# Performance work log

Hardware: AMD Instinct MI355X
Metric: run time of the kernel (lower is better)

Reference implementation:

```python
import jax, jax.numpy as jnp
import numpy as np

N_NODES = 50000
N_EDGES = 1600000
D_FEAT = 512
FILTERS = 256
NUM_CLASSES = 16


def setup_inputs() -> dict:
    key = jax.random.key(0)
    k = jax.random.split(key, 6)
    x = jax.random.normal(k[0], (N_NODES, D_FEAT), dtype=jnp.float32)
    W1 = jax.random.normal(k[1], (D_FEAT, FILTERS), dtype=jnp.float32) * (1.0 / np.sqrt(D_FEAT))
    W2 = jax.random.normal(k[2], (FILTERS, NUM_CLASSES), dtype=jnp.float32) * (1.0 / np.sqrt(FILTERS))
    edge_weight = jax.random.uniform(k[3], (N_EDGES,), dtype=jnp.float32)
    edge_src = jax.random.randint(k[4], (N_EDGES,), 0, N_NODES, dtype=jnp.int32)
    edge_dst = jax.random.randint(k[5], (N_EDGES,), 0, N_NODES, dtype=jnp.int32)
    return {"x": x, "W1": W1, "W2": W2, "edge_weight": edge_weight,
            "edge_src": edge_src, "edge_dst": edge_dst}


def _propagate(h, edge_src, edge_dst, edge_weight):
    # sparse A @ h: out[dst] += w * h[src]
    msgs = edge_weight[:, None] * h[edge_src]          # [E, F]
    return jax.ops.segment_sum(msgs, edge_dst, num_segments=N_NODES)


def reference(x, W1, W2, edge_weight, edge_src, edge_dst):
    # Dropout layers are identity at inference (training=False).
    # Layer 1: relu(A @ (X @ W1))
    h = jax.nn.relu(_propagate(x @ W1, edge_src, edge_dst, edge_weight))
    # Layer 2: softmax(A @ (H @ W2))
    logits = _propagate(h @ W2, edge_src, edge_dst, edge_weight)
    return jax.nn.softmax(logits, axis=-1)
```

## Files before the change

kernel.cpp:

```cpp
#include <hip/hip_runtime.h>

#define N_NODES 50000
#define N_EDGES 1600000
#define D_FEAT 512
#define FILTERS 256
#define NUM_CLASSES 16
#define NXCD 8

typedef __bf16 bf16x8 __attribute__((ext_vector_type(8)));
typedef float f32x4 __attribute__((ext_vector_type(4)));
typedef _Float16 half4 __attribute__((ext_vector_type(4)));
typedef _Float16 f16x8 __attribute__((ext_vector_type(8)));

#define GLOAD_LDS16(g, l)                                                  \
  __builtin_amdgcn_global_load_lds(                                        \
      (const __attribute__((address_space(1))) unsigned int*)(g),          \
      (__attribute__((address_space(3))) unsigned int*)(l), 16, 0, 0)

__global__ __launch_bounds__(256) void hist8_kernel(
    const int* __restrict__ edst, int* __restrict__ deg8) {
  const int e = blockIdx.x * 256 + threadIdx.x;
  if (e >= N_EDGES) return;
  const int x = blockIdx.x & (NXCD - 1);
  atomicAdd(&deg8[x * N_NODES + edst[e]], 1);
}

#define SCAN_NB 196
__global__ __launch_bounds__(256) void scan_blocks_kernel(
    const int* __restrict__ deg8, int* __restrict__ row_ptr,
    int* __restrict__ bsum, const float* __restrict__ W1,
    __bf16* __restrict__ Wth, __bf16* __restrict__ Wtl) {
  const int gtid = blockIdx.x * 256 + threadIdx.x;
  for (int i = gtid; i < D_FEAT * FILTERS; i += SCAN_NB * 256) {
    const float v = W1[i];
    const int k = i >> 8;
    const int n = i & 255;
    const __bf16 h = (__bf16)v;
    Wth[n * D_FEAT + k] = h;
    Wtl[n * D_FEAT + k] = (__bf16)(v - (float)h);
  }

  __shared__ int s[256];
  const int i = gtid;
  int v = 0;
  if (i < N_NODES) {
#pragma unroll
    for (int x = 0; x < NXCD; ++x) v += deg8[x * N_NODES + i];
  }
  s[threadIdx.x] = v;
  __syncthreads();
  for (int off = 1; off < 256; off <<= 1) {
    const int t = (threadIdx.x >= off) ? s[threadIdx.x - off] : 0;
    __syncthreads();
    s[threadIdx.x] += t;
    __syncthreads();
  }
  if (i < N_NODES) row_ptr[i] = s[threadIdx.x] - v;
  if (threadIdx.x == 255) bsum[blockIdx.x] = s[255];
}

__global__ __launch_bounds__(256) void scan_add_cursor8_kernel(
    int* __restrict__ row_ptr, const int* __restrict__ bsum,
    const int* __restrict__ deg8, int* __restrict__ cursor8) {
  __shared__ int wsum[4];
  const int lane = threadIdx.x & 63;
  const int wave = threadIdx.x >> 6;
  int v = (threadIdx.x < blockIdx.x) ? bsum[threadIdx.x] : 0;
#pragma unroll
  for (int off = 32; off >= 1; off >>= 1) v += __shfl_xor(v, off, 64);
  if (lane == 0) wsum[wave] = v;
  __syncthreads();
  const int boff = wsum[0] + wsum[1] + wsum[2] + wsum[3];

  const int i = blockIdx.x * 256 + threadIdx.x;
  if (i < N_NODES) {
    int run = row_ptr[i] + boff;
    row_ptr[i] = run;
#pragma unroll
    for (int x = 0; x < NXCD; ++x) {
      cursor8[x * N_NODES + i] = run;
      run += deg8[x * N_NODES + i];
    }
  }
  if (i == 0) row_ptr[N_NODES] = N_EDGES;
}

__global__ __launch_bounds__(256) void fill8_kernel(
    const int* __restrict__ esrc, const int* __restrict__ edst,
    const float* __restrict__ ew, int* __restrict__ cursor8,
    uint2* __restrict__ meta8) {
  const int e = blockIdx.x * 256 + threadIdx.x;
  if (e >= N_EDGES) return;
  const int x = blockIdx.x & (NXCD - 1);
  const int d = edst[e];
  const int pos = atomicAdd(&cursor8[x * N_NODES + d], 1);
  meta8[pos] = make_uint2((unsigned)esrc[e] | ((unsigned)(d & 15) << 16),
                          __float_as_uint(ew[e]));
}

__global__ __launch_bounds__(256) void gemm1_mfma_kernel(
    const float* __restrict__ A, const __bf16* __restrict__ Bh,
    const __bf16* __restrict__ Bl, _Float16* __restrict__ C) {
  const int K = D_FEAT;
  __shared__ __bf16 sAh[128 * 32];
  __shared__ __bf16 sAl[128 * 32];
  __shared__ __bf16 sBh[128 * 32];
  __shared__ __bf16 sBl[128 * 32];

  const int tid = threadIdx.x;
  const int wave = tid >> 6;
  const int lane = tid & 63;
  const int wm = (wave >> 1) * 64;
  const int wn = (wave & 1) * 64;
  const int m0 = blockIdx.x * 128;
  const int n0 = blockIdx.y * 128;

  const int arow = tid >> 1;
  const int aks = (tid & 1) * 16;
  int am = m0 + arow;
  if (am >= N_NODES) am = N_NODES - 1;
  const float* aptr = A + (size_t)am * K + aks;

  const int lr = lane >> 2;
  const int lc = (lane & 3) * 8;
  const int fm = lane & 15;
  const int fq = lane >> 4;

  f32x4 acc[4][4] = {};

  for (int k0 = 0; k0 < K; k0 += 32) {
    const float4* ap = (const float4*)(aptr + k0);
    const float4 a0 = ap[0], a1 = ap[1], a2 = ap[2], a3 = ap[3];

    __syncthreads();

#pragma unroll
    for (int i = 0; i < 2; ++i) {
      const int row = wave * 32 + i * 16;
      GLOAD_LDS16(Bh + (size_t)(n0 + row + lr) * K + k0 + lc, sBh + row * 32);
      GLOAD_LDS16(Bl + (size_t)(n0 + row + lr) * K + k0 + lc, sBl + row * 32);
    }

    float va[16] = {a0.x, a0.y, a0.z, a0.w, a1.x, a1.y, a1.z, a1.w,
                    a2.x, a2.y, a2.z, a2.w, a3.x, a3.y, a3.z, a3.w};
    __bf16 hh[16], ll[16];
#pragma unroll
    for (int i = 0; i < 16; ++i) {
      const __bf16 h = (__bf16)va[i];
      hh[i] = h;
      ll[i] = (__bf16)(va[i] - (float)h);
    }
    *(bf16x8*)(sAh + arow * 32 + aks) = *(bf16x8*)&hh[0];
    *(bf16x8*)(sAh + arow * 32 + aks + 8) = *(bf16x8*)&hh[8];
    *(bf16x8*)(sAl + arow * 32 + aks) = *(bf16x8*)&ll[0];
    *(bf16x8*)(sAl + arow * 32 + aks + 8) = *(bf16x8*)&ll[8];

    __syncthreads();

    bf16x8 fah[4], fal[4], fbh[4], fbl[4];
#pragma unroll
    for (int t = 0; t < 4; ++t) {
      const int moff = (wm + t * 16 + fm) * 32 + fq * 8;
      fah[t] = *(const bf16x8*)(sAh + moff);
      fal[t] = *(const bf16x8*)(sAl + moff);
      const int noff = (wn + t * 16 + fm) * 32 + fq * 8;
      fbh[t] = *(const bf16x8*)(sBh + noff);
      fbl[t] = *(const bf16x8*)(sBl + noff);
    }
#pragma unroll
    for (int i = 0; i < 4; ++i)
#pragma unroll
      for (int j = 0; j < 4; ++j)
        acc[i][j] = __builtin_amdgcn_mfma_f32_16x16x32_bf16(fah[i], fbh[j],
                                                            acc[i][j], 0, 0, 0);
#pragma unroll
    for (int i = 0; i < 4; ++i)
#pragma unroll
      for (int j = 0; j < 4; ++j)
        acc[i][j] = __builtin_amdgcn_mfma_f32_16x16x32_bf16(fah[i], fbl[j],
                                                            acc[i][j], 0, 0, 0);
#pragma unroll
    for (int i = 0; i < 4; ++i)
#pragma unroll
      for (int j = 0; j < 4; ++j)
        acc[i][j] = __builtin_amdgcn_mfma_f32_16x16x32_bf16(fal[i], fbh[j],
                                                            acc[i][j], 0, 0, 0);
  }

#pragma unroll
  for (int ti = 0; ti < 4; ++ti) {
#pragma unroll
    for (int r = 0; r < 4; ++r) {
      const int m = m0 + wm + ti * 16 + fq * 4 + r;
      if (m < N_NODES) {
#pragma unroll
        for (int tj = 0; tj < 4; ++tj) {
          const int n = n0 + wn + tj * 16 + fm;
          C[(size_t)m * FILTERS + n] = (_Float16)acc[ti][tj][r];
        }
      }
    }
  }
}

__global__ __launch_bounds__(256) void gather1_gemm2_kernel(
    const _Float16* __restrict__ xw1, const int* __restrict__ row_ptr,
    const uint2* __restrict__ meta8, const float* __restrict__ W2,
    _Float16* __restrict__ h2) {
  __shared__ float red[4][16][17];
  const int wave = threadIdx.x >> 6;
  const int lane = threadIdx.x & 63;
  const int node = blockIdx.x * 4 + wave;
  const int beg = row_ptr[node];
  const int end = row_ptr[node + 1];

  float acc[4] = {};
  const half4* __restrict__ xw1v = (const half4*)xw1;

  for (int c0 = beg; c0 < end; c0 += 64) {
    const int cnt = min(64, end - c0);
    const uint2 mv = meta8[c0 + ((lane < cnt) ? lane : 0)];

    for (int j = 0; j < cnt; j += 8) {
      int srcs[8];
      float ws[8];
#pragma unroll
      for (int u = 0; u < 8; ++u) {
        const int live = (j + u < cnt);
        const int l = live ? (j + u) : 0;
        srcs[u] = __builtin_amdgcn_readlane((int)mv.x, l) & 0xFFFF;
        const int wb = __builtin_amdgcn_readlane((int)mv.y, l);
        ws[u] = live ? __int_as_float(wb) : 0.f;
      }
      half4 v[8];
#pragma unroll
      for (int u = 0; u < 8; ++u)
        v[u] = xw1v[(unsigned)srcs[u] * 64u + (unsigned)lane];
#pragma unroll
      for (int u = 0; u < 8; ++u)
#pragma unroll
        for (int i = 0; i < 4; ++i)
          acc[i] = fmaf(ws[u], (float)v[u][i], acc[i]);
    }
  }

  float r[4];
#pragma unroll
  for (int i = 0; i < 4; ++i) r[i] = fmaxf(acc[i], 0.f);

  float p[16] = {};
#pragma unroll
  for (int j = 0; j < 4; ++j) {
    const float4* wr = (const float4*)(W2 + (size_t)(lane * 4 + j) * NUM_CLASSES);
#pragma unroll
    for (int c4 = 0; c4 < 4; ++c4) {
      const float4 wv = wr[c4];
      p[c4 * 4 + 0] = fmaf(r[j], wv.x, p[c4 * 4 + 0]);
      p[c4 * 4 + 1] = fmaf(r[j], wv.y, p[c4 * 4 + 1]);
      p[c4 * 4 + 2] = fmaf(r[j], wv.z, p[c4 * 4 + 2]);
      p[c4 * 4 + 3] = fmaf(r[j], wv.w, p[c4 * 4 + 3]);
    }
  }

#pragma unroll
  for (int off = 32; off >= 16; off >>= 1)
#pragma unroll
    for (int i = 0; i < 16; ++i) p[i] += __shfl_xor(p[i], off, 64);

  if (lane < 16) {
#pragma unroll
    for (int i = 0; i < 16; ++i) red[wave][lane][i] = p[i];
  }
  if (lane < 16) {
    float sum = 0.f;
#pragma unroll
    for (int i = 0; i < 16; ++i) sum += red[wave][i][lane];
    h2[(size_t)node * NUM_CLASSES + lane] = (_Float16)sum;
  }
}

__global__ __launch_bounds__(256) void gather2_mfma_kernel(
    const _Float16* __restrict__ h2, const int* __restrict__ row_ptr,
    const uint2* __restrict__ meta8, float* __restrict__ out) {
  __shared__ _Float16 lds[4][16][72];
  const int wave = threadIdx.x >> 6;
  const int lane = threadIdx.x & 63;
  const int tile = blockIdx.x * 4 + wave;
  if (tile >= N_NODES / 16) return;
  const int t0 = tile * 16;
  const int beg = row_ptr[t0];
  const int end = row_ptr[t0 + 16];

  const int cls = lane & 15;
  const int kq = lane >> 4;
  const int erow = lane >> 1;
  const int part = lane & 1;

  f32x4 acc = {0.f, 0.f, 0.f, 0.f};
  _Float16* myl = &lds[wave][0][0];

  if (beg < end) {
    const int last = end - 1;
    int e = beg + lane;
    uint2 m = meta8[(e <= last) ? e : last];
    float wv = (e <= last) ? __uint_as_float(m.y) : 0.f;

    for (int c0 = beg; c0 < end; c0 += 64) {
      uint2 mn = m;
      float wn = 0.f;
      const int c1 = c0 + 64;
      if (c1 < end) {
        const int en = c1 + lane;
        mn = meta8[(en <= last) ? en : last];
        wn = (en <= last) ? __uint_as_float(mn.y) : 0.f;
      }

      const int se0 = __shfl((int)m.x, erow, 64) & 0xFFFF;
      const int se1 = __shfl((int)m.x, 32 + erow, 64) & 0xFFFF;
      const f16x8 r0 =
          *(const f16x8*)(h2 + (size_t)se0 * NUM_CLASSES + part * 8);
      const f16x8 r1 =
          *(const f16x8*)(h2 + (size_t)se1 * NUM_CLASSES + part * 8);

      f16x8 a0, a1;
#pragma unroll
      for (int j = 0; j < 8; ++j) {
        const int ei = kq * 8 + j;
        const int p0 = __shfl((int)m.x, ei, 64);
        const float w0 = __shfl(wv, ei, 64);
        a0[j] = (((p0 >> 16) & 15) == cls) ? (_Float16)w0 : (_Float16)0.f;
        const int p1 = __shfl((int)m.x, 32 + ei, 64);
        const float w1 = __shfl(wv, 32 + ei, 64);
        a1[j] = (((p1 >> 16) & 15) == cls) ? (_Float16)w1 : (_Float16)0.f;
      }

#pragma unroll
      for (int j = 0; j < 8; ++j) myl[(part * 8 + j) * 72 + erow] = r0[j];
#pragma unroll
      for (int j = 0; j < 8; ++j) myl[(part * 8 + j) * 72 + 32 + erow] = r1[j];

      const f16x8 b0 = *(const f16x8*)(myl + cls * 72 + kq * 8);
      const f16x8 b1 = *(const f16x8*)(myl + cls * 72 + 32 + kq * 8);

      acc = __builtin_amdgcn_mfma_f32_16x16x32_f16(a0, b0, acc, 0, 0, 0);
      acc = __builtin_amdgcn_mfma_f32_16x16x32_f16(a1, b1, acc, 0, 0, 0);

      m = mn;
      wv = wn;
    }
  }

#pragma unroll
  for (int r = 0; r < 4; ++r) {
    const float a = acc[r];
    float mx = a;
#pragma unroll
    for (int off = 8; off >= 1; off >>= 1)
      mx = fmaxf(mx, __shfl_xor(mx, off, 16));
    const float ex = __expf(a - mx);
    float sm = ex;
#pragma unroll
    for (int off = 8; off >= 1; off >>= 1) sm += __shfl_xor(sm, off, 16);
    out[(size_t)(t0 + kq * 4 + r) * NUM_CLASSES + cls] = ex / sm;
  }
}

extern "C" void kernel_launch(void* const* d_in, const int* in_sizes, int n_in,
                              void* d_out, int out_size, void* d_ws,
                              size_t ws_size, hipStream_t stream) {
  const float* x = (const float*)d_in[0];
  const float* W1 = (const float*)d_in[1];
  const float* W2 = (const float*)d_in[2];
  const float* ew = (const float*)d_in[3];
  const int* esrc = (const int*)d_in[4];
  const int* edst = (const int*)d_in[5];
  float* out = (float*)d_out;

  _Float16* xw1 = (_Float16*)d_ws;
  _Float16* h2 = xw1 + (size_t)N_NODES * FILTERS;
  int* row_ptr = (int*)(h2 + (size_t)N_NODES * NUM_CLASSES);
  int* deg8 = row_ptr + (N_NODES + 1);
  int* cursor8 = deg8 + NXCD * N_NODES;
  uint2* meta8 = (uint2*)(((uintptr_t)(cursor8 + NXCD * N_NODES) + 15) &
                          ~(uintptr_t)15);
  __bf16* w1th = (__bf16*)(meta8 + N_EDGES);
  __bf16* w1tl = w1th + D_FEAT * FILTERS;
  int* bsum = (int*)(w1tl + D_FEAT * FILTERS);

  hipMemsetAsync(deg8, 0, NXCD * N_NODES * sizeof(int), stream);
  hist8_kernel<<<(N_EDGES + 255) / 256, 256, 0, stream>>>(edst, deg8);
  scan_blocks_kernel<<<SCAN_NB, 256, 0, stream>>>(deg8, row_ptr, bsum, W1,
                                                  w1th, w1tl);
  scan_add_cursor8_kernel<<<SCAN_NB, 256, 0, stream>>>(row_ptr, bsum, deg8,
                                                       cursor8);
  fill8_kernel<<<(N_EDGES + 255) / 256, 256, 0, stream>>>(esrc, edst, ew,
                                                          cursor8, meta8);

  dim3 g1((N_NODES + 127) / 128, FILTERS / 128);
  gemm1_mfma_kernel<<<g1, 256, 0, stream>>>(x, w1th, w1tl, xw1);

  gather1_gemm2_kernel<<<N_NODES / 4, 256, 0, stream>>>(xw1, row_ptr, meta8,
                                                        W2, h2);

  gather2_mfma_kernel<<<(N_NODES / 16 + 3) / 4, 256, 0, stream>>>(h2, row_ptr,
                                                                  meta8, out);
}
```

Baseline: 544.6 us.

## Fuse CSR fill into GEMM1 launch and move W1 split into histogram kernel

Merges the edge fill (CSR scatter) kernel into the GEMM1 kernel as extra blocks, so the atomic-heavy fill runs concurrently with the MFMA GEMM instead of serially, and cuts one launch. The W1 bf16 hi/lo transpose-split moves from the scan kernel into the histogram kernel, so the scan kernels become lighter. The XCD bucket index now comes from the edge index rather than blockIdx. Fill blocks share the GEMM's LDS allocation, which may lower occupancy for them, and scheduling order decides how much overlap actually happens.

New measurement: 489.7 us. 1.11x faster.

```diff
diff --git a/kernel.cpp b/kernel.cpp
--- a/kernel.cpp
+++ b/kernel.cpp
@@ -18,30 +18,29 @@
       (__attribute__((address_space(3))) unsigned int*)(l), 16, 0, 0)
 
 __global__ __launch_bounds__(256) void hist8_kernel(
-    const int* __restrict__ edst, int* __restrict__ deg8) {
+    const int* __restrict__ edst, int* __restrict__ deg8,
+    const float* __restrict__ W1, __bf16* __restrict__ Wth,
+    __bf16* __restrict__ Wtl) {
   const int e = blockIdx.x * 256 + threadIdx.x;
+  if (e < D_FEAT * FILTERS) {
+    const float v = W1[e];
+    const int k = e >> 8;
+    const int n = e & 255;
+    const __bf16 h = (__bf16)v;
+    Wth[n * D_FEAT + k] = h;
+    Wtl[n * D_FEAT + k] = (__bf16)(v - (float)h);
+  }
   if (e >= N_EDGES) return;
-  const int x = blockIdx.x & (NXCD - 1);
+  const int x = (e >> 8) & (NXCD - 1);
   atomicAdd(&deg8[x * N_NODES + edst[e]], 1);
 }
 
 #define SCAN_NB 196
 __global__ __launch_bounds__(256) void scan_blocks_kernel(
     const int* __restrict__ deg8, int* __restrict__ row_ptr,
-    int* __restrict__ bsum, const float* __restrict__ W1,
-    __bf16* __restrict__ Wth, __bf16* __restrict__ Wtl) {
-  const int gtid = blockIdx.x * 256 + threadIdx.x;
-  for (int i = gtid; i < D_FEAT * FILTERS; i += SCAN_NB * 256) {
-    const float v = W1[i];
-    const int k = i >> 8;
-    const int n = i & 255;
-    const __bf16 h = (__bf16)v;
-    Wth[n * D_FEAT + k] = h;
-    Wtl[n * D_FEAT + k] = (__bf16)(v - (float)h);
-  }
-
+    int* __restrict__ bsum) {
   __shared__ int s[256];
-  const int i = gtid;
+  const int i = blockIdx.x * 256 + threadIdx.x;
   int v = 0;
   if (i < N_NODES) {
 #pragma unroll
@@ -85,35 +84,39 @@
   if (i == 0) row_ptr[N_NODES] = N_EDGES;
 }
 
-__global__ __launch_bounds__(256) void fill8_kernel(
+#define G1_BX 391
+#define G1_BLOCKS (G1_BX * 2)
+__global__ __launch_bounds__(256) void gemm1_fill_kernel(
+    const float* __restrict__ A, const __bf16* __restrict__ Bh,
+    const __bf16* __restrict__ Bl, _Float16* __restrict__ C,
     const int* __restrict__ esrc, const int* __restrict__ edst,
     const float* __restrict__ ew, int* __restrict__ cursor8,
     uint2* __restrict__ meta8) {
-  const int e = blockIdx.x * 256 + threadIdx.x;
-  if (e >= N_EDGES) return;
-  const int x = blockIdx.x & (NXCD - 1);
-  const int d = edst[e];
-  const int pos = atomicAdd(&cursor8[x * N_NODES + d], 1);
-  meta8[pos] = make_uint2((unsigned)esrc[e] | ((unsigned)(d & 15) << 16),
-                          __float_as_uint(ew[e]));
-}
-
-__global__ __launch_bounds__(256) void gemm1_mfma_kernel(
-    const float* __restrict__ A, const __bf16* __restrict__ Bh,
-    const __bf16* __restrict__ Bl, _Float16* __restrict__ C) {
-  const int K = D_FEAT;
   __shared__ __bf16 sAh[128 * 32];
   __shared__ __bf16 sAl[128 * 32];
   __shared__ __bf16 sBh[128 * 32];
   __shared__ __bf16 sBl[128 * 32];
 
+  if (blockIdx.x >= G1_BLOCKS) {
+    const int e = (blockIdx.x - G1_BLOCKS) * 256 + threadIdx.x;
+    if (e < N_EDGES) {
+      const int x = (e >> 8) & (NXCD - 1);
+      const int d = edst[e];
+      const int pos = atomicAdd(&cursor8[x * N_NODES + d], 1);
+      meta8[pos] = make_uint2((unsigned)esrc[e] | ((unsigned)(d & 15) << 16),
+                              __float_as_uint(ew[e]));
+    }
+    return;
+  }
+
+  const int K = D_FEAT;
   const int tid = threadIdx.x;
   const int wave = tid >> 6;
   const int lane = tid & 63;
   const int wm = (wave >> 1) * 64;
   const int wn = (wave & 1) * 64;
-  const int m0 = blockIdx.x * 128;
-  const int n0 = blockIdx.y * 128;
+  const int m0 = (blockIdx.x % G1_BX) * 128;
+  const int n0 = (blockIdx.x / G1_BX) * 128;
 
   const int arow = tid >> 1;
   const int aks = (tid & 1) * 16;
@@ -388,16 +391,14 @@
   int* bsum = (int*)(w1tl + D_FEAT * FILTERS);
 
   hipMemsetAsync(deg8, 0, NXCD * N_NODES * sizeof(int), stream);
-  hist8_kernel<<<(N_EDGES + 255) / 256, 256, 0, stream>>>(edst, deg8);
-  scan_blocks_kernel<<<SCAN_NB, 256, 0, stream>>>(deg8, row_ptr, bsum, W1,
-                                                  w1th, w1tl);
+  hist8_kernel<<<(N_EDGES + 255) / 256, 256, 0, stream>>>(edst, deg8, W1,
+                                                          w1th, w1tl);
+  scan_blocks_kernel<<<SCAN_NB, 256, 0, stream>>>(deg8, row_ptr, bsum);
   scan_add_cursor8_kernel<<<SCAN_NB, 256, 0, stream>>>(row_ptr, bsum, deg8,
                                                        cursor8);
-  fill8_kernel<<<(N_EDGES + 255) / 256, 256, 0, stream>>>(esrc, edst, ew,
-                                                          cursor8, meta8);
-
-  dim3 g1((N_NODES + 127) / 128, FILTERS / 128);
-  gemm1_mfma_kernel<<<g1, 256, 0, stream>>>(x, w1th, w1tl, xw1);
+
+  gemm1_fill_kernel<<<G1_BLOCKS + (N_EDGES + 255) / 256, 256, 0, stream>>>(
+      x, w1th, w1tl, xw1, esrc, edst, ew, cursor8, meta8);
 
   gather1_gemm2_kernel<<<N_NODES / 4, 256, 0, stream>>>(xw1, row_ptr, meta8,
                                                         W2, h2);
```
